# Performance work log

Hardware: AMD Instinct MI355X
Metric: run time of the kernel (lower is better)

The kernel has to match this reference:

```python
import jax, jax.numpy as jnp
import numpy as np

B, T, C, H = 2, 2048, 2048, 16  # batch, seq_len, dim, num_heads
D = C // H  # head_dim = 128
ROPE_BASE = 10000.0


def apply_rope(x, pos):
    # x: [B, T, H, D]; adjacent-pair rotation (torchtune convention)
    d = x.shape[-1]
    inv_freq = 1.0 / (ROPE_BASE ** (jnp.arange(0, d, 2, dtype=jnp.float32) / d))  # [D/2]
    freqs = pos.astype(jnp.float32)[:, None] * inv_freq[None, :]                 # [T, D/2]
    cos = jnp.cos(freqs)[None, :, None, :]
    sin = jnp.sin(freqs)[None, :, None, :]
    x1 = x[..., 0::2]
    x2 = x[..., 1::2]
    out = jnp.stack([x1 * cos - x2 * sin, x2 * cos + x1 * sin], axis=-1)  # [B,T,H,D/2,2]
    return out.reshape(x.shape)


def setup_inputs() -> dict:
    key = jax.random.key(0)
    k1, k2, k3 = jax.random.split(key, 3)
    x = jax.random.normal(k1, (B, T, C), dtype=jnp.float32)
    # 0.02 init scale keeps attention logits in a sane range
    W_qkv = jax.random.normal(k2, (C, 3 * C), dtype=jnp.float32) * 0.02
    W_out = jax.random.normal(k3, (C, C), dtype=jnp.float32) * 0.02
    return {"x": x, "W_qkv": W_qkv, "W_out": W_out}


def reference(x, W_qkv, W_out):
    b, t, c = x.shape
    h, d = H, c // H
    # fused QKV projection
    qkv = (x @ W_qkv).reshape(b, t, 3, h, d)
    q, k, v = qkv[:, :, 0], qkv[:, :, 1], qkv[:, :, 2]  # [B,T,H,D] each
    pos = jnp.arange(t)  # cache_pos = 0 (prefill)
    q = apply_rope(q, pos)
    k = apply_rope(k, pos)
    scale = 1.0 / np.sqrt(d).astype(np.float32)
    scores = jnp.einsum('bqhd,bkhd->bhqk', q, k) * scale  # [B,H,T,T]
    causal = jnp.tril(jnp.ones((t, t), dtype=bool))
    scores = jnp.where(causal[None, None], scores, -jnp.inf)
    probs = jax.nn.softmax(scores, axis=-1)
    o = jnp.einsum('bhqk,bkhd->bqhd', probs, v).reshape(b, t, c)
    return o @ W_out
```

## Files before the change

kernel.cpp:

```cpp
#include <hip/hip_runtime.h>
#include <stdint.h>

#define TSEQ 2048

typedef __bf16 bf16x8 __attribute__((ext_vector_type(8)));
typedef float f32x4 __attribute__((ext_vector_type(4)));

typedef const __attribute__((address_space(1))) unsigned int* gas_u32;
typedef __attribute__((address_space(3))) unsigned int* las_u32;

__device__ __forceinline__ f32x4 mfma16(bf16x8 a, bf16x8 b, f32x4 c) {
  return __builtin_amdgcn_mfma_f32_16x16x32_bf16(a, b, c, 0, 0, 0);
}

__device__ __forceinline__ unsigned short f2b(float f) {
  unsigned int u = __float_as_uint(f);
  u += 0x7fffu + ((u >> 16) & 1u);
  return (unsigned short)(u >> 16);
}

__device__ __forceinline__ void gload_lds16(const unsigned short* g, unsigned short* l) {
  __builtin_amdgcn_global_load_lds((gas_u32)(const void*)g, (las_u32)(void*)l, 16, 0, 0);
}

__global__ __launch_bounds__(256) void cast_bf16_kernel(const float* __restrict__ src,
                                                        unsigned short* __restrict__ dst) {
  size_t i = ((size_t)blockIdx.x * 256 + threadIdx.x) * 4;
  float4 v = *(const float4*)(src + i);
  ushort4 o;
  o.x = f2b(v.x); o.y = f2b(v.y); o.z = f2b(v.z); o.w = f2b(v.w);
  *(ushort4*)(dst + i) = o;
}

__global__ __launch_bounds__(256) void transpose_cast_kernel(const float* __restrict__ src,
                                                             unsigned short* __restrict__ dst,
                                                             int R, int Cc) {
  __shared__ float tile[64][65];
  int cb = blockIdx.x * 64;
  int rb = blockIdx.y * 64;
  int t = threadIdx.x;
  int tr = t >> 4;
  int tc = (t & 15) * 4;
#pragma unroll
  for (int i = 0; i < 4; i++) {
    int r = tr + 16 * i;
    float4 v = *(const float4*)(src + (size_t)(rb + r) * Cc + cb + tc);
    tile[r][tc + 0] = v.x; tile[r][tc + 1] = v.y;
    tile[r][tc + 2] = v.z; tile[r][tc + 3] = v.w;
  }
  __syncthreads();
#pragma unroll
  for (int i = 0; i < 4; i++) {
    int r2 = tr + 16 * i;
    ushort4 o;
    o.x = f2b(tile[tc + 0][r2]);
    o.y = f2b(tile[tc + 1][r2]);
    o.z = f2b(tile[tc + 2][r2]);
    o.w = f2b(tile[tc + 3][r2]);
    *(ushort4*)(dst + (size_t)(cb + r2) * R + rb + tc) = o;
  }
}

__device__ __forceinline__ void gemm_bt_core_db(const unsigned short* __restrict__ A,
                                                const unsigned short* __restrict__ Bt,
                                                int K, int bm, int bn,
                                                unsigned short* sm,
                                                f32x4 (&acc)[4][4]) {
  const int t = threadIdx.x;
  const int lane = t & 63, w = t >> 6;
  const int wm = (w >> 1) * 64, wn = (w & 1) * 64;
  const int quad = lane >> 4, l16 = lane & 15;

  const int r0 = t >> 2;
  const int s0 = (((t & 3) ^ ((r0 >> 1) & 3)) * 8);
  const unsigned short* Arow0 = A + (size_t)(bm + r0) * K + s0;
  const unsigned short* Arow1 = Arow0 + (size_t)64 * K;
  const unsigned short* Brow0 = Bt + (size_t)(bn + r0) * K + s0;
  const unsigned short* Brow1 = Brow0 + (size_t)64 * K;

  auto stage = [&](int k0, int buf) {
    unsigned short* sA = sm + buf * 8192;
    unsigned short* sB = sA + 4096;
    gload_lds16(Arow0 + k0, sA + t * 8);
    gload_lds16(Arow1 + k0, sA + (t + 256) * 8);
    gload_lds16(Brow0 + k0, sB + t * 8);
    gload_lds16(Brow1 + k0, sB + (t + 256) * 8);
  };

  const int sw = (l16 >> 1) & 3;
  stage(0, 0);
  const int nIter = K >> 5;
#pragma unroll 1
  for (int it = 0; it < nIter; it++) {
    __syncthreads();
    if (it + 1 < nIter) stage((it + 1) * 32, (it + 1) & 1);
    const unsigned short* sA = sm + (it & 1) * 8192;
    const unsigned short* sB = sA + 4096;
    bf16x8 a[4], b[4];
#pragma unroll
    for (int i = 0; i < 4; i++)
      a[i] = *(const bf16x8*)(sA + (wm + i * 16 + l16) * 32 + ((quad ^ sw) * 8));
#pragma unroll
    for (int j = 0; j < 4; j++)
      b[j] = *(const bf16x8*)(sB + (wn + j * 16 + l16) * 32 + ((quad ^ sw) * 8));
#pragma unroll
    for (int i = 0; i < 4; i++)
#pragma unroll
      for (int j = 0; j < 4; j++)
        acc[i][j] = mfma16(a[i], b[j], acc[i][j]);
  }
  __syncthreads();
}

__global__ __launch_bounds__(256, 3) void gemm_qkv_rope(const unsigned short* __restrict__ Xb,
                                                        const unsigned short* __restrict__ Wqt,
                                                        unsigned short* __restrict__ Qd,
                                                        unsigned short* __restrict__ Kd,
                                                        unsigned short* __restrict__ Vtd) {
  __shared__ unsigned short smem[24576];
  f32x4 acc[4][4];
  const f32x4 z = {0.f, 0.f, 0.f, 0.f};
#pragma unroll
  for (int i = 0; i < 4; i++)
#pragma unroll
    for (int j = 0; j < 4; j++) acc[i][j] = z;

  const int bm = blockIdx.y * 128;
  const int bnb = blockIdx.x;
  gemm_bt_core_db(Xb, Wqt, 2048, bm, bnb * 128, smem, acc);

  const int s = bnb >> 4, h = bnb & 15;
  const int t = threadIdx.x, lane = t & 63, w = t >> 6;
  const int wm = (w >> 1) * 64, wn = (w & 1) * 64;
  const int quad = lane >> 4, l16 = lane & 15;
  const int bq = bm >> 11;
  const int tpos0 = bm & (TSEQ - 1);
  unsigned short* sC = smem;

  if (s < 2) {
    const float scl = (s == 0) ? 0.08838834764831845f : 1.0f;
#pragma unroll
    for (int j = 0; j < 4; j++) {
      int d = wn + j * 16 + l16;
      float invf = __expf(-(float)(d >> 1) * 0.14391157f);
#pragma unroll
      for (int i = 0; i < 4; i++) {
#pragma unroll
        for (int r = 0; r < 4; r++) {
          int row = wm + i * 16 + quad * 4 + r;
          float ang = (float)(tpos0 + row) * invf;
          float sn, cs;
          __sincosf(ang, &sn, &cs);
          float v = acc[i][j][r];
          float p = __shfl_xor(v, 1, 64);
          float outv = (d & 1) ? (v * cs + p * sn) : (v * cs - p * sn);
          sC[row * 136 + d] = f2b(outv * scl);
        }
      }
    }
    __syncthreads();
    unsigned short* dst = (s == 0) ? Qd : Kd;
    size_t gbase = ((size_t)(bq * 16 + h) * TSEQ + tpos0) * 128;
#pragma unroll
    for (int it = 0; it < 8; it++) {
      int c = t + 256 * it;
      int row = c >> 4, off = (c & 15) * 8;
      uint4 vv = *(const uint4*)(sC + row * 136 + off);
      *(uint4*)(dst + gbase + (size_t)row * 128 + off) = vv;
    }
  } else {
#pragma unroll
    for (int j = 0; j < 4; j++) {
      int d = wn + j * 16 + l16;
#pragma unroll
      for (int i = 0; i < 4; i++)
#pragma unroll
        for (int r = 0; r < 4; r++) {
          int col = wm + i * 16 + quad * 4 + r;
          sC[d * 136 + col] = f2b(acc[i][j][r]);
        }
    }
    __syncthreads();
    size_t gbase = ((size_t)(bq * 16 + h) * 128) * TSEQ + tpos0;
#pragma unroll
    for (int it = 0; it < 8; it++) {
      int c = t + 256 * it;
      int row = c >> 4, off = (c & 15) * 8;
      uint4 vv = *(const uint4*)(sC + row * 136 + off);
      *(uint4*)(Vtd + gbase + (size_t)row * TSEQ + off) = vv;
    }
  }
}

__global__ __launch_bounds__(256, 2) void attn_kernel(const unsigned short* __restrict__ Q,
                                                      const unsigned short* __restrict__ Kmat,
                                                      const unsigned short* __restrict__ Vt,
                                                      unsigned short* __restrict__ Ob) {
  __shared__ unsigned short smem[37376];
  const int pair = blockIdx.x, bh = blockIdx.y;
  const int qA = pair, qB = 31 - pair;
  const int t = threadIdx.x, lane = t & 63, w = t >> 6, quad = lane >> 4, l16 = lane & 15;
  const size_t base = (size_t)bh * TSEQ * 128;
  const unsigned short* Qp = Q + base;
  const unsigned short* Kp = Kmat + base;
  const unsigned short* Vp = Vt + base;
  unsigned short* myP = smem + 32768 + w * 1152;

  bf16x8 aqA[4], aqB[4];
  {
    int qrA = qA * 64 + w * 16 + l16;
    int qrB = qB * 64 + w * 16 + l16;
#pragma unroll
    for (int kk = 0; kk < 4; kk++) {
      aqA[kk] = *(const bf16x8*)(Qp + (size_t)qrA * 128 + kk * 32 + quad * 8);
      aqB[kk] = *(const bf16x8*)(Qp + (size_t)qrB * 128 + kk * 32 + quad * 8);
    }
  }
  const f32x4 z = {0.f, 0.f, 0.f, 0.f};
  f32x4 oA[8], oB[8];
  float mA[4], lA[4], mB[4], lB[4];
#pragma unroll
  for (int dt = 0; dt < 8; dt++) { oA[dt] = z; oB[dt] = z; }
#pragma unroll
  for (int r = 0; r < 4; r++) { mA[r] = -1e30f; lA[r] = 0.f; mB[r] = -1e30f; lB[r] = 0.f; }

  auto load_tiles = [&](int kb, int buf) {
    unsigned short* bK = smem + buf * 16384;
    unsigned short* bV = bK + 8192;
    const unsigned short* Kt = Kp + (size_t)kb * 64 * 128;
#pragma unroll
    for (int i2 = 0; i2 < 4; i2++) {
      int idx = t + 256 * i2;
      int r = idx >> 4, cS = idx & 15;
      int c = cS ^ (r & 7);
      gload_lds16(Kt + r * 128 + c * 8, bK + idx * 8);
    }
#pragma unroll
    for (int i2 = 0; i2 < 4; i2++) {
      int idx = t + 256 * i2;
      int r = idx >> 3, cS = idx & 7;
      int c = cS ^ (r & 7);
      gload_lds16(Vp + (size_t)r * TSEQ + kb * 64 + c * 8, bV + idx * 8);
    }
  };

  auto process = [&](bf16x8 (&aq)[4], f32x4 (&o)[8], float (&mst)[4], float (&lst)[4],
                     int qb, int kb, const unsigned short* bK, const unsigned short* bV) {
    f32x4 S[4];
#pragma unroll
    for (int nt = 0; nt < 4; nt++) {
      f32x4 sacc = z;
#pragma unroll
      for (int kk = 0; kk < 4; kk++) {
        const unsigned short* p =
            bK + (nt * 16 + l16) * 128 + (((kk * 4 + quad) ^ (l16 & 7)) * 8);
        sacc = mfma16(aq[kk], *(const bf16x8*)p, sacc);
      }
      S[nt] = sacc;
    }
    if (kb == qb) {
      int qg = qb * 64 + w * 16 + quad * 4;
#pragma unroll
      for (int nt = 0; nt < 4; nt++) {
        int key = kb * 64 + nt * 16 + l16;
#pragma unroll
        for (int r = 0; r < 4; r++)
          if (key > qg + r) S[nt][r] = -1e30f;
      }
    }
    float alpha[4];
#pragma unroll
    for (int r = 0; r < 4; r++) {
      float mx = fmaxf(fmaxf(S[0][r], S[1][r]), fmaxf(S[2][r], S[3][r]));
      mx = fmaxf(mx, __shfl_xor(mx, 1, 64));
      mx = fmaxf(mx, __shfl_xor(mx, 2, 64));
      mx = fmaxf(mx, __shfl_xor(mx, 4, 64));
      mx = fmaxf(mx, __shfl_xor(mx, 8, 64));
      float mnew = fmaxf(mst[r], mx);
      alpha[r] = __expf(mst[r] - mnew);
      mst[r] = mnew;
    }
    float rs[4] = {0.f, 0.f, 0.f, 0.f};
#pragma unroll
    for (int nt = 0; nt < 4; nt++)
#pragma unroll
      for (int r = 0; r < 4; r++) {
        float p = __expf(S[nt][r] - mst[r]);
        S[nt][r] = p;
        rs[r] += p;
      }
#pragma unroll
    for (int r = 0; r < 4; r++) {
      float s4 = rs[r];
      s4 += __shfl_xor(s4, 1, 64);
      s4 += __shfl_xor(s4, 2, 64);
      s4 += __shfl_xor(s4, 4, 64);
      s4 += __shfl_xor(s4, 8, 64);
      lst[r] = lst[r] * alpha[r] + s4;
#pragma unroll
      for (int nt = 0; nt < 4; nt++)
        myP[(quad * 4 + r) * 72 + nt * 16 + l16] = f2b(S[nt][r]);
    }
#pragma unroll
    for (int dt = 0; dt < 8; dt++) {
      f32x4 ov = o[dt];
      ov[0] *= alpha[0]; ov[1] *= alpha[1]; ov[2] *= alpha[2]; ov[3] *= alpha[3];
      o[dt] = ov;
    }
#pragma unroll
    for (int kk = 0; kk < 2; kk++) {
      bf16x8 ap = *(const bf16x8*)(myP + l16 * 72 + kk * 32 + quad * 8);
#pragma unroll
      for (int dt = 0; dt < 8; dt++) {
        const unsigned short* p =
            bV + (dt * 16 + l16) * 64 + (((kk * 4 + quad) ^ (l16 & 7)) * 8);
        o[dt] = mfma16(ap, *(const bf16x8*)p, o[dt]);
      }
    }
  };

  load_tiles(0, 0);
#pragma unroll 1
  for (int kb = 0; kb <= qB; kb++) {
    __syncthreads();
    if (kb < qB) load_tiles(kb + 1, (kb + 1) & 1);
    const unsigned short* bK = smem + (kb & 1) * 16384;
    const unsigned short* bV = bK + 8192;
    process(aqB, oB, mB, lB, qB, kb, bK, bV);
    if (kb <= qA) process(aqA, oA, mA, lA, qA, kb, bK, bV);
  }

  __syncthreads();
  unsigned short* sOA = smem;
  unsigned short* sOB = smem + 8704;
#pragma unroll
  for (int dt = 0; dt < 8; dt++)
#pragma unroll
    for (int r = 0; r < 4; r++) {
      int row = w * 16 + quad * 4 + r;
      sOA[row * 136 + dt * 16 + l16] = f2b(oA[dt][r] / lA[r]);
      sOB[row * 136 + dt * 16 + l16] = f2b(oB[dt][r] / lB[r]);
    }
  __syncthreads();
  const int b = bh >> 4, h = bh & 15;
#pragma unroll
  for (int it = 0; it < 4; it++) {
    int c = t + 256 * it;
    int row = c >> 4, off = (c & 15) * 8;
    uint4 va = *(const uint4*)(sOA + row * 136 + off);
    *(uint4*)(Ob + (size_t)(b * TSEQ + qA * 64 + row) * 2048 + h * 128 + off) = va;
    uint4 vb = *(const uint4*)(sOB + row * 136 + off);
    *(uint4*)(Ob + (size_t)(b * TSEQ + qB * 64 + row) * 2048 + h * 128 + off) = vb;
  }
}

__global__ __launch_bounds__(256, 4) void gemm_out_kernel(const unsigned short* __restrict__ Ob,
                                                          const unsigned short* __restrict__ Wot,
                                                          float* __restrict__ Cout) {
  __shared__ unsigned short smem[16384];
  f32x4 acc[4][4];
  const f32x4 z = {0.f, 0.f, 0.f, 0.f};
#pragma unroll
  for (int i = 0; i < 4; i++)
#pragma unroll
    for (int j = 0; j < 4; j++) acc[i][j] = z;

  const int bm = blockIdx.y * 128, bn = blockIdx.x * 128;
  gemm_bt_core_db(Ob, Wot, 2048, bm, bn, smem, acc);

  const int t = threadIdx.x, lane = t & 63, w = t >> 6;
  const int wm = (w >> 1) * 64, wn = (w & 1) * 64;
  const int quad = lane >> 4, l16 = lane & 15;
#pragma unroll
  for (int i = 0; i < 4; i++)
#pragma unroll
    for (int j = 0; j < 4; j++)
#pragma unroll
      for (int r = 0; r < 4; r++) {
        int row = bm + wm + i * 16 + quad * 4 + r;
        int col = bn + wn + j * 16 + l16;
        Cout[(size_t)row * 2048 + col] = acc[i][j][r];
      }
}

extern "C" void kernel_launch(void* const* d_in, const int* in_sizes, int n_in,
                              void* d_out, int out_size, void* d_ws, size_t ws_size,
                              hipStream_t stream) {
  (void)in_sizes; (void)n_in; (void)out_size; (void)ws_size;
  const float* x = (const float*)d_in[0];
  const float* Wqkv = (const float*)d_in[1];
  const float* Wout = (const float*)d_in[2];
  float* out = (float*)d_out;
  char* ws = (char*)d_ws;

  unsigned short* Xb  = (unsigned short*)(ws);
  unsigned short* Wqt = (unsigned short*)(ws + 16777216);
  unsigned short* Wot = (unsigned short*)(ws + 41943040);
  unsigned short* Qd  = (unsigned short*)(ws + 50331648);
  unsigned short* Kd  = (unsigned short*)(ws + 67108864);
  unsigned short* Vtd = (unsigned short*)(ws + 83886080);
  unsigned short* Obf = (unsigned short*)(ws + 100663296);

  cast_bf16_kernel<<<8192, 256, 0, stream>>>(x, Xb);
  transpose_cast_kernel<<<dim3(96, 32), 256, 0, stream>>>(Wqkv, Wqt, 2048, 6144);
  transpose_cast_kernel<<<dim3(32, 32), 256, 0, stream>>>(Wout, Wot, 2048, 2048);
  gemm_qkv_rope<<<dim3(48, 32), 256, 0, stream>>>(Xb, Wqt, Qd, Kd, Vtd);
  attn_kernel<<<dim3(16, 32), 256, 0, stream>>>(Qd, Kd, Vtd, Obf);
  gemm_out_kernel<<<dim3(16, 32), 256, 0, stream>>>(Obf, Wot, out);
}
```

Measured before the change: 387.8 us.

## Rework GEMM core to 128x256 tiles with triple-buffered K=64 stages

Replaces the double-buffered 128x128, K=32 GEMM core with a 512-thread 128x256 tile core that uses K=64 steps, three LDS stages, and explicit vmcnt waits. Global-to-LDS staging is interleaved with MFMA groups under s_setprio. The goal is to hide load latency better and raise reuse per LDS load in the QKV and output projections. The epilogues are adapted to write two heads per block. In exchange, each block uses much more LDS (about 144KB), which limits occupancy. The grids also shrink to 768 and 256 blocks, which may underfill the CUs.

```diff
diff --git a/kernel.cpp b/kernel.cpp
--- a/kernel.cpp
+++ b/kernel.cpp
@@ -61,63 +61,117 @@
   }
 }
 
-__device__ __forceinline__ void gemm_bt_core_db(const unsigned short* __restrict__ A,
-                                                const unsigned short* __restrict__ Bt,
-                                                int K, int bm, int bn,
-                                                unsigned short* sm,
-                                                f32x4 (&acc)[4][4]) {
+__device__ __forceinline__ void gemm_core_256(const unsigned short* __restrict__ A,
+                                              const unsigned short* __restrict__ Bt,
+                                              int K, int bm, int bn,
+                                              unsigned short* sm,
+                                              f32x4 (&acc)[4][4]) {
   const int t = threadIdx.x;
   const int lane = t & 63, w = t >> 6;
-  const int wm = (w >> 1) * 64, wn = (w & 1) * 64;
+  const int wm = (w >> 2) * 64;
+  const int wn = (w & 3) * 64;
   const int quad = lane >> 4, l16 = lane & 15;
-
-  const int r0 = t >> 2;
-  const int s0 = (((t & 3) ^ ((r0 >> 1) & 3)) * 8);
-  const unsigned short* Arow0 = A + (size_t)(bm + r0) * K + s0;
-  const unsigned short* Arow1 = Arow0 + (size_t)64 * K;
-  const unsigned short* Brow0 = Bt + (size_t)(bn + r0) * K + s0;
-  const unsigned short* Brow1 = Brow0 + (size_t)64 * K;
-
-  auto stage = [&](int k0, int buf) {
-    unsigned short* sA = sm + buf * 8192;
-    unsigned short* sB = sA + 4096;
-    gload_lds16(Arow0 + k0, sA + t * 8);
-    gload_lds16(Arow1 + k0, sA + (t + 256) * 8);
-    gload_lds16(Brow0 + k0, sB + t * 8);
-    gload_lds16(Brow1 + k0, sB + (t + 256) * 8);
+  const int rsw = l16 & 7;
+
+  const int srow = t >> 3;
+  const int gch = (t & 7) ^ (srow & 7);
+  const unsigned short* pA = A + (size_t)(bm + srow) * K + gch * 8;
+  const unsigned short* pB = Bt + (size_t)(bn + srow) * K + gch * 8;
+  const size_t K64 = (size_t)64 * K;
+
+  auto stageA = [&](int k0, unsigned short* dstSlot) {
+    gload_lds16(pA + k0, dstSlot + t * 8);
+    gload_lds16(pA + K64 + k0, dstSlot + (t + 512) * 8);
   };
-
-  const int sw = (l16 >> 1) & 3;
-  stage(0, 0);
-  const int nIter = K >> 5;
+  auto stageB01 = [&](int k0, unsigned short* dstSlot) {
+    unsigned short* tB = dstSlot + 8192;
+    gload_lds16(pB + k0, tB + t * 8);
+    gload_lds16(pB + K64 + k0, tB + (t + 512) * 8);
+  };
+  auto stageB23 = [&](int k0, unsigned short* dstSlot) {
+    unsigned short* tB = dstSlot + 8192;
+    gload_lds16(pB + 2 * K64 + k0, tB + (t + 1024) * 8);
+    gload_lds16(pB + 3 * K64 + k0, tB + (t + 1536) * 8);
+  };
+
+  stageA(0, sm);          stageB01(0, sm);          stageB23(0, sm);
+  stageA(64, sm + 24576); stageB01(64, sm + 24576); stageB23(64, sm + 24576);
+
+  const int nIter = K >> 6;
+  int scur = 0, sstg = 2;
+
 #pragma unroll 1
   for (int it = 0; it < nIter; it++) {
-    __syncthreads();
-    if (it + 1 < nIter) stage((it + 1) * 32, (it + 1) & 1);
-    const unsigned short* sA = sm + (it & 1) * 8192;
-    const unsigned short* sB = sA + 4096;
-    bf16x8 a[4], b[4];
-#pragma unroll
-    for (int i = 0; i < 4; i++)
-      a[i] = *(const bf16x8*)(sA + (wm + i * 16 + l16) * 32 + ((quad ^ sw) * 8));
-#pragma unroll
-    for (int j = 0; j < 4; j++)
-      b[j] = *(const bf16x8*)(sB + (wn + j * 16 + l16) * 32 + ((quad ^ sw) * 8));
-#pragma unroll
-    for (int i = 0; i < 4; i++)
-#pragma unroll
-      for (int j = 0; j < 4; j++)
-        acc[i][j] = mfma16(a[i], b[j], acc[i][j]);
+    if (it + 1 < nIter)
+      asm volatile("s_waitcnt vmcnt(6) lgkmcnt(0)" ::: "memory");
+    else
+      asm volatile("s_waitcnt vmcnt(0) lgkmcnt(0)" ::: "memory");
+    __builtin_amdgcn_s_barrier();
+    asm volatile("" ::: "memory");
+
+    const unsigned short* sA = sm + scur * 24576;
+    const unsigned short* sB = sA + 8192;
+    unsigned short* tgt = sm + sstg * 24576;
+    const bool doStage = (it + 2 < nIter);
+    const int k2 = (it + 2) << 6;
+
+    bf16x8 aF[2][2], b0[2][2], b1[2][2];
+
+    auto mm8 = [&](int ib, int jb, bf16x8 (&af)[2][2], bf16x8 (&bf)[2][2]) {
+      __builtin_amdgcn_s_setprio(1);
+#pragma unroll
+      for (int i2 = 0; i2 < 2; i2++)
+#pragma unroll
+        for (int j2 = 0; j2 < 2; j2++)
+#pragma unroll
+          for (int kk = 0; kk < 2; kk++)
+            acc[ib + i2][jb + j2] = mfma16(af[i2][kk], bf[j2][kk], acc[ib + i2][jb + j2]);
+      __builtin_amdgcn_s_setprio(0);
+    };
+
+#pragma unroll
+    for (int i2 = 0; i2 < 2; i2++)
+#pragma unroll
+      for (int kk = 0; kk < 2; kk++)
+        aF[i2][kk] = *(const bf16x8*)(sA + (wm + i2 * 16 + l16) * 64 + (((kk * 4 + quad) ^ rsw) * 8));
+#pragma unroll
+    for (int j2 = 0; j2 < 2; j2++)
+#pragma unroll
+      for (int kk = 0; kk < 2; kk++)
+        b0[j2][kk] = *(const bf16x8*)(sB + (wn + j2 * 16 + l16) * 64 + (((kk * 4 + quad) ^ rsw) * 8));
+    if (doStage) stageA(k2, tgt);
+    mm8(0, 0, aF, b0);
+
+#pragma unroll
+    for (int j2 = 0; j2 < 2; j2++)
+#pragma unroll
+      for (int kk = 0; kk < 2; kk++)
+        b1[j2][kk] = *(const bf16x8*)(sB + (wn + (2 + j2) * 16 + l16) * 64 + (((kk * 4 + quad) ^ rsw) * 8));
+    if (doStage) stageB01(k2, tgt);
+    mm8(0, 2, aF, b1);
+
+#pragma unroll
+    for (int i2 = 0; i2 < 2; i2++)
+#pragma unroll
+      for (int kk = 0; kk < 2; kk++)
+        aF[i2][kk] = *(const bf16x8*)(sA + (wm + (2 + i2) * 16 + l16) * 64 + (((kk * 4 + quad) ^ rsw) * 8));
+    if (doStage) stageB23(k2, tgt);
+    mm8(2, 2, aF, b1);
+
+    mm8(2, 0, aF, b0);
+
+    scur = (scur == 2) ? 0 : scur + 1;
+    sstg = (sstg == 2) ? 0 : sstg + 1;
   }
   __syncthreads();
 }
 
-__global__ __launch_bounds__(256, 3) void gemm_qkv_rope(const unsigned short* __restrict__ Xb,
+__global__ __launch_bounds__(512, 2) void gemm_qkv_rope(const unsigned short* __restrict__ Xb,
                                                         const unsigned short* __restrict__ Wqt,
                                                         unsigned short* __restrict__ Qd,
                                                         unsigned short* __restrict__ Kd,
                                                         unsigned short* __restrict__ Vtd) {
-  __shared__ unsigned short smem[24576];
+  __shared__ unsigned short smem[73728];
   f32x4 acc[4][4];
   const f32x4 z = {0.f, 0.f, 0.f, 0.f};
 #pragma unroll
@@ -126,12 +180,14 @@
     for (int j = 0; j < 4; j++) acc[i][j] = z;
 
   const int bm = blockIdx.y * 128;
-  const int bnb = blockIdx.x;
-  gemm_bt_core_db(Xb, Wqt, 2048, bm, bnb * 128, smem, acc);
-
-  const int s = bnb >> 4, h = bnb & 15;
+  const int bn = blockIdx.x * 256;
+  gemm_core_256(Xb, Wqt, 2048, bm, bn, smem, acc);
+
+  const int c0 = blockIdx.x * 2;
+  const int s = c0 >> 4;
+  const int hA = c0 & 15, hB = (c0 + 1) & 15;
   const int t = threadIdx.x, lane = t & 63, w = t >> 6;
-  const int wm = (w >> 1) * 64, wn = (w & 1) * 64;
+  const int wm = (w >> 2) * 64, wn = (w & 3) * 64;
   const int quad = lane >> 4, l16 = lane & 15;
   const int bq = bm >> 11;
   const int tpos0 = bm & (TSEQ - 1);
@@ -142,7 +198,8 @@
 #pragma unroll
     for (int j = 0; j < 4; j++) {
       int d = wn + j * 16 + l16;
-      float invf = __expf(-(float)(d >> 1) * 0.14391157f);
+      int dh = d & 127;
+      float invf = __expf(-(float)(dh >> 1) * 0.14391157f);
 #pragma unroll
       for (int i = 0; i < 4; i++) {
 #pragma unroll
@@ -154,19 +211,19 @@
           float v = acc[i][j][r];
           float p = __shfl_xor(v, 1, 64);
           float outv = (d & 1) ? (v * cs + p * sn) : (v * cs - p * sn);
-          sC[row * 136 + d] = f2b(outv * scl);
+          sC[row * 264 + d] = f2b(outv * scl);
         }
       }
     }
     __syncthreads();
     unsigned short* dst = (s == 0) ? Qd : Kd;
-    size_t gbase = ((size_t)(bq * 16 + h) * TSEQ + tpos0) * 128;
 #pragma unroll
     for (int it = 0; it < 8; it++) {
-      int c = t + 256 * it;
-      int row = c >> 4, off = (c & 15) * 8;
-      uint4 vv = *(const uint4*)(sC + row * 136 + off);
-      *(uint4*)(dst + gbase + (size_t)row * 128 + off) = vv;
+      int u = t + 512 * it;
+      int row = u >> 5, cc = u & 31;
+      int hl = cc >> 4;
+      size_t gb = ((size_t)(bq * 16 + (hl ? hB : hA)) * TSEQ + tpos0 + row) * 128 + (cc & 15) * 8;
+      *(uint4*)(dst + gb) = *(const uint4*)(sC + row * 264 + cc * 8);
     }
   } else {
 #pragma unroll
@@ -181,13 +238,13 @@
         }
     }
     __syncthreads();
-    size_t gbase = ((size_t)(bq * 16 + h) * 128) * TSEQ + tpos0;
 #pragma unroll
     for (int it = 0; it < 8; it++) {
-      int c = t + 256 * it;
-      int row = c >> 4, off = (c & 15) * 8;
-      uint4 vv = *(const uint4*)(sC + row * 136 + off);
-      *(uint4*)(Vtd + gbase + (size_t)row * TSEQ + off) = vv;
+      int u = t + 512 * it;
+      int dd = u >> 4, cc = u & 15;
+      int hl = dd >> 7, dl = dd & 127;
+      size_t gb = ((size_t)(bq * 16 + (hl ? hB : hA)) * 128 + dl) * TSEQ + tpos0 + cc * 8;
+      *(uint4*)(Vtd + gb) = *(const uint4*)(sC + dd * 136 + cc * 8);
     }
   }
 }
@@ -354,10 +411,10 @@
   }
 }
 
-__global__ __launch_bounds__(256, 4) void gemm_out_kernel(const unsigned short* __restrict__ Ob,
+__global__ __launch_bounds__(512, 2) void gemm_out_kernel(const unsigned short* __restrict__ Ob,
                                                           const unsigned short* __restrict__ Wot,
                                                           float* __restrict__ Cout) {
-  __shared__ unsigned short smem[16384];
+  __shared__ unsigned short smem[73728];
   f32x4 acc[4][4];
   const f32x4 z = {0.f, 0.f, 0.f, 0.f};
 #pragma unroll
@@ -365,11 +422,11 @@
 #pragma unroll
     for (int j = 0; j < 4; j++) acc[i][j] = z;
 
-  const int bm = blockIdx.y * 128, bn = blockIdx.x * 128;
-  gemm_bt_core_db(Ob, Wot, 2048, bm, bn, smem, acc);
+  const int bm = blockIdx.y * 128, bn = blockIdx.x * 256;
+  gemm_core_256(Ob, Wot, 2048, bm, bn, smem, acc);
 
   const int t = threadIdx.x, lane = t & 63, w = t >> 6;
-  const int wm = (w >> 1) * 64, wn = (w & 1) * 64;
+  const int wm = (w >> 2) * 64, wn = (w & 3) * 64;
   const int quad = lane >> 4, l16 = lane & 15;
 #pragma unroll
   for (int i = 0; i < 4; i++)
@@ -404,7 +461,7 @@
   cast_bf16_kernel<<<8192, 256, 0, stream>>>(x, Xb);
   transpose_cast_kernel<<<dim3(96, 32), 256, 0, stream>>>(Wqkv, Wqt, 2048, 6144);
   transpose_cast_kernel<<<dim3(32, 32), 256, 0, stream>>>(Wout, Wot, 2048, 2048);
-  gemm_qkv_rope<<<dim3(48, 32), 256, 0, stream>>>(Xb, Wqt, Qd, Kd, Vtd);
+  gemm_qkv_rope<<<dim3(24, 32), 512, 0, stream>>>(Xb, Wqt, Qd, Kd, Vtd);
   attn_kernel<<<dim3(16, 32), 256, 0, stream>>>(Qd, Kd, Vtd, Obf);
-  gemm_out_kernel<<<dim3(16, 32), 256, 0, stream>>>(Obf, Wot, out);
-}
+  gemm_out_kernel<<<dim3(8, 32), 512, 0, stream>>>(Obf, Wot, out);
+}
```

Result: faster. 374.5 us (-3.4%).
